# Kernel tuning notes

Hardware: AMD Instinct MI355X
Metric: run time of the kernel (lower is better)

Reference implementation:

```python
import jax, jax.numpy as jnp
import numpy as np

N_NODES = 100000
N_EDGES = 1600000
IN_FT = 128
OUT_FT = 128


def setup_inputs() -> dict:
    key = jax.random.key(0)
    k1, k2, k3, k4, k5, k6 = jax.random.split(key, 6)
    stdv = 1.0 / np.sqrt(OUT_FT)
    x = jax.random.normal(k1, (N_NODES, IN_FT), dtype=jnp.float32)
    edge_rows = jax.random.randint(k2, (N_EDGES,), 0, N_NODES, dtype=jnp.int32)
    edge_cols = jax.random.randint(k3, (N_EDGES,), 0, N_NODES, dtype=jnp.int32)
    # normalized adjacency values (positive, like D^-1 A)
    edge_vals = jax.random.uniform(k4, (N_EDGES,), dtype=jnp.float32)
    W = jax.random.uniform(k5, (IN_FT, OUT_FT), dtype=jnp.float32, minval=-stdv, maxval=stdv)
    b = jax.random.uniform(k6, (OUT_FT,), dtype=jnp.float32, minval=-stdv, maxval=stdv)
    return {"x": x, "edge_rows": edge_rows, "edge_cols": edge_cols,
            "edge_vals": edge_vals, "W": W, "b": b}


def reference(x, edge_rows, edge_cols, edge_vals, W, b):
    # dense projection + bias: [N, out_ft]
    h = x @ W + b
    # SpMM: out[r] = sum_e vals[e] * h[cols[e]] for edges with rows[e] == r
    msgs = edge_vals[:, None] * h[edge_cols]          # [E, out_ft]
    out = jax.ops.segment_sum(msgs, edge_rows, num_segments=N_NODES)
    return jax.nn.relu(out)
```

## Files before the change

kernel.cpp:

```cpp
#include <hip/hip_runtime.h>

#define N_NODES 100000
#define N_EDGES 1600000
#define FT 128

#define NBUCK 391
#define EPB 4096
#define NBLKP ((N_EDGES + EPB - 1) / EPB)
#define CAP 1536
#define CAPB 4800
#define OVFCAP 65536
#define GEMM_BLOCKS ((N_NODES + 255) / 256)
#define SPMM_GRID (8 * 4 * ((NBUCK + 7) / 8))

#define OFF_H 0
#define OFF_BUCKETED 25600000
#define OFF_GCUR 40614400
#define OFF_NOVF 40615964
#define OFF_OVFREC 40615968
#define OFF_OVFBUCK 41140256
#define WS_NEEDED 41402400

typedef __attribute__((ext_vector_type(8))) short bf16x8;
typedef __attribute__((ext_vector_type(4))) float f32x4;

static __device__ __forceinline__ ushort f2bf(float f) {
  const unsigned u = __float_as_uint(f);
  return (ushort)((u + 0x7FFF + ((u >> 16) & 1)) >> 16);
}
static __device__ __forceinline__ float bf2f(ushort s) {
  return __uint_as_float((unsigned)s << 16);
}

__global__ __launch_bounds__(256) void fused_gemm_partC_kernel(
    const float* __restrict__ x,
    const float* __restrict__ W,
    const float* __restrict__ b,
    ushort* __restrict__ h,
    const int* __restrict__ erows,
    const int* __restrict__ ecols,
    const float* __restrict__ evals,
    int* gcur,
    int* novf,
    int2* __restrict__ ovf_rec,
    int* __restrict__ ovf_buck,
    int2* __restrict__ bucketed) {
  __shared__ __align__(16) ushort whi[16384];
  __shared__ int cnt[NBUCK];
  const int tid = threadIdx.x;

  if (blockIdx.x < GEMM_BLOCKS) {
    for (int idx = tid; idx < 16384; idx += 256) {
      const int k = idx >> 7;
      const int col = idx & 127;
      const ushort hi = f2bf(W[idx]);
      const int lane_ = (((k >> 3) & 3) << 4) | (col & 15);
      const int pos =
          ((((k >> 5) << 3) + (col >> 4)) * 64 + lane_) * 8 + (k & 7);
      whi[pos] = hi;
    }
    __syncthreads();

    const int w = tid >> 6;
    const int lane = tid & 63;
    const int r0 = blockIdx.x * 256 + w * 64;
    const int arow = lane & 15;
    const int kgrp = (lane >> 4) << 3;

    float bias_v[8];
#pragma unroll
    for (int ct = 0; ct < 8; ++ct) bias_v[ct] = b[ct * 16 + (lane & 15)];

    f32x4 acc[4][8];
#pragma unroll
    for (int rf = 0; rf < 4; ++rf)
#pragma unroll
      for (int ct = 0; ct < 8; ++ct) acc[rf][ct] = (f32x4){0.f, 0.f, 0.f, 0.f};

#pragma unroll
    for (int ks = 0; ks < 4; ++ks) {
      bf16x8 afr[4];
#pragma unroll
      for (int rf = 0; rf < 4; ++rf) {
        int r = r0 + rf * 16 + arow;
        r = (r < N_NODES) ? r : (N_NODES - 1);
        const float* xp = x + (size_t)r * FT + ks * 32 + kgrp;
        const float4 u0 = *(const float4*)xp;
        const float4 u1 = *(const float4*)(xp + 4);
        bf16x8 a;
        a[0] = (short)f2bf(u0.x);
        a[1] = (short)f2bf(u0.y);
        a[2] = (short)f2bf(u0.z);
        a[3] = (short)f2bf(u0.w);
        a[4] = (short)f2bf(u1.x);
        a[5] = (short)f2bf(u1.y);
        a[6] = (short)f2bf(u1.z);
        a[7] = (short)f2bf(u1.w);
        afr[rf] = a;
      }
#pragma unroll
      for (int ct = 0; ct < 8; ++ct) {
        const int fo = ((ks * 8 + ct) * 64 + lane) * 8;
        const bf16x8 bh = *(const bf16x8*)&whi[fo];
#pragma unroll
        for (int rf = 0; rf < 4; ++rf) {
          acc[rf][ct] = __builtin_amdgcn_mfma_f32_16x16x32_bf16(
              afr[rf], bh, acc[rf][ct], 0, 0, 0);
        }
      }
    }

    const int crow0 = (lane >> 4) << 2;
    const int ccol = lane & 15;
#pragma unroll
    for (int rf = 0; rf < 4; ++rf) {
#pragma unroll
      for (int ct = 0; ct < 8; ++ct) {
        const int col = ct * 16 + ccol;
#pragma unroll
        for (int i = 0; i < 4; ++i) {
          const int row = r0 + rf * 16 + crow0 + i;
          if (row < N_NODES)
            h[(size_t)row * FT + col] = f2bf(acc[rf][ct][i] + bias_v[ct]);
        }
      }
    }
  } else {
    const int bid = blockIdx.x - GEMM_BLOCKS;
    for (int j = tid; j < NBUCK; j += 256) cnt[j] = 0;
    __syncthreads();

    const int base4 = bid * (EPB / 4);
#pragma unroll
    for (int it = 0; it < EPB / 4 / 256; ++it) {
      const int idx4 = base4 + it * 256 + tid;
      if (idx4 < N_EDGES / 4) {
        const int4 r = ((const int4*)erows)[idx4];
        atomicAdd(&cnt[r.x >> 8], 1);
        atomicAdd(&cnt[r.y >> 8], 1);
        atomicAdd(&cnt[r.z >> 8], 1);
        atomicAdd(&cnt[r.w >> 8], 1);
      }
    }
    __syncthreads();

    for (int j = tid; j < NBUCK; j += 256) {
      const int hj = cnt[j];
      int base = 0;
      if (hj > 0) base = atomicAdd(&gcur[j], hj);
      cnt[j] = j * CAPB + ((base < CAPB) ? base : CAPB);
    }
    __syncthreads();

#pragma unroll
    for (int it = 0; it < EPB / 4 / 256; ++it) {
      const int idx4 = base4 + it * 256 + tid;
      if (idx4 < N_EDGES / 4) {
        const int4 r = ((const int4*)erows)[idx4];
        const int4 c = ((const int4*)ecols)[idx4];
        const float4 v = ((const float4*)evals)[idx4];
        int bb, p, lim;
        int2 rec;
#define SCAT(RR, CC, VV)                                           \
        bb = (RR) >> 8;                                            \
        rec.x = (((RR) & 255) << 24) | (CC);                       \
        rec.y = __float_as_int(VV);                                \
        p = atomicAdd(&cnt[bb], 1);                                \
        lim = bb * CAPB + CAPB;                                    \
        if (p < lim) {                                             \
          bucketed[p] = rec;                                       \
        } else {                                                   \
          const int op = atomicAdd(novf, 1);                       \
          if (op < OVFCAP) { ovf_rec[op] = rec; ovf_buck[op] = bb; } \
        }
        SCAT(r.x, c.x, v.x)
        SCAT(r.y, c.y, v.y)
        SCAT(r.z, c.z, v.z)
        SCAT(r.w, c.w, v.w)
#undef SCAT
      }
    }
  }
}

__global__ __launch_bounds__(512) void spmm_bucket_kernel(
    const int2* __restrict__ bucketed,
    const int* __restrict__ gcur,
    const int* __restrict__ novf,
    const int2* __restrict__ ovf_rec,
    const int* __restrict__ ovf_buck,
    const ushort* __restrict__ h,
    float* __restrict__ out) {
  __shared__ int2 tmp[CAP];
  __shared__ int2 eds[CAP];
  __shared__ int cnt[64];
  __shared__ int pos[64];
  __shared__ int cur[64];
  __shared__ int ns;
  const int p_ = blockIdx.x;
  const int x_ = p_ & 7;
  const int m_ = p_ >> 3;
  const int q = m_ & 3;
  const int b = 8 * (m_ >> 2) + x_;
  if (b >= NBUCK) return;
  const int t = threadIdx.x;
  const int beg = b * CAPB;
  const int fill = gcur[b];
  const int end = beg + ((fill < CAPB) ? fill : CAPB);
  const int nov = *novf;

  if (t < 64) cnt[t] = 0;
  if (t == 0) ns = 0;
  __syncthreads();

  for (int i = beg + t; i < end; i += 512) {
    const int2 rec = bucketed[i];
    const int r8 = ((unsigned)rec.x) >> 24;
    if ((r8 >> 6) == q) {
      const int p = atomicAdd(&ns, 1);
      if (p < CAP) {
        tmp[p] = rec;
        atomicAdd(&cnt[r8 & 63], 1);
      }
    }
  }
  __syncthreads();

  const int m = (ns < CAP) ? ns : CAP;
  const bool overflow = (ns > CAP);

  if (t < 64) pos[t] = cnt[t];
  __syncthreads();
#pragma unroll
  for (int d = 1; d < 64; d <<= 1) {
    int u = 0;
    if (t < 64 && t >= d) u = pos[t - d];
    __syncthreads();
    if (t < 64) pos[t] += u;
    __syncthreads();
  }
  if (t < 64) {
    const int excl = pos[t] - cnt[t];
    pos[t] = excl;
    cur[t] = excl;
  }
  __syncthreads();

  for (int i = t; i < m; i += 512) {
    const int2 rec = tmp[i];
    const int r6 = (((unsigned)rec.x) >> 24) & 63;
    const int p = atomicAdd(&cur[r6], 1);
    eds[p] = (int2){rec.x & 0x00FFFFFF, rec.y};
  }
  __syncthreads();

  const int g = t >> 5;
  const int lane = t & 31;
  const int j = lane * 4;

  for (int rr = 0; rr < 4; ++rr) {
    const int r = rr * 16 + g;
    const int row = b * 256 + q * 64 + r;
    const int rbeg = pos[r];
    const int rend = cur[r];

    float a0 = 0.f, a1 = 0.f, a2 = 0.f, a3 = 0.f;
    int e = rbeg;
    for (; e + 3 < rend; e += 4) {
      const int2 p0 = eds[e];
      const int2 p1 = eds[e + 1];
      const int2 p2 = eds[e + 2];
      const int2 p3 = eds[e + 3];
      const ushort4 q0 = *(const ushort4*)(h + (size_t)p0.x * FT + j);
      const ushort4 q1 = *(const ushort4*)(h + (size_t)p1.x * FT + j);
      const ushort4 q2 = *(const ushort4*)(h + (size_t)p2.x * FT + j);
      const ushort4 q3 = *(const ushort4*)(h + (size_t)p3.x * FT + j);
      const float v0 = __int_as_float(p0.y);
      const float v1 = __int_as_float(p1.y);
      const float v2 = __int_as_float(p2.y);
      const float v3 = __int_as_float(p3.y);
      a0 = fmaf(v0, bf2f(q0.x), a0);
      a1 = fmaf(v0, bf2f(q0.y), a1);
      a2 = fmaf(v0, bf2f(q0.z), a2);
      a3 = fmaf(v0, bf2f(q0.w), a3);
      a0 = fmaf(v1, bf2f(q1.x), a0);
      a1 = fmaf(v1, bf2f(q1.y), a1);
      a2 = fmaf(v1, bf2f(q1.z), a2);
      a3 = fmaf(v1, bf2f(q1.w), a3);
      a0 = fmaf(v2, bf2f(q2.x), a0);
      a1 = fmaf(v2, bf2f(q2.y), a1);
      a2 = fmaf(v2, bf2f(q2.z), a2);
      a3 = fmaf(v2, bf2f(q2.w), a3);
      a0 = fmaf(v3, bf2f(q3.x), a0);
      a1 = fmaf(v3, bf2f(q3.y), a1);
      a2 = fmaf(v3, bf2f(q3.z), a2);
      a3 = fmaf(v3, bf2f(q3.w), a3);
    }
    for (; e < rend; ++e) {
      const int2 p0 = eds[e];
      const float v0 = __int_as_float(p0.y);
      const ushort4 q0 = *(const ushort4*)(h + (size_t)p0.x * FT + j);
      a0 = fmaf(v0, bf2f(q0.x), a0);
      a1 = fmaf(v0, bf2f(q0.y), a1);
      a2 = fmaf(v0, bf2f(q0.z), a2);
      a3 = fmaf(v0, bf2f(q0.w), a3);
    }
    if (overflow) {
      int seen = 0;
      const int have = rend - rbeg;
      for (int i = beg; i < end; ++i) {
        const int2 rec = bucketed[i];
        const int r8 = ((unsigned)rec.x) >> 24;
        if ((r8 >> 6) == q && (r8 & 63) == r) {
          ++seen;
          if (seen > have) {
            const float v0 = __int_as_float(rec.y);
            const ushort4 q0 =
                *(const ushort4*)(h + (size_t)(rec.x & 0x00FFFFFF) * FT + j);
            a0 = fmaf(v0, bf2f(q0.x), a0);
            a1 = fmaf(v0, bf2f(q0.y), a1);
            a2 = fmaf(v0, bf2f(q0.z), a2);
            a3 = fmaf(v0, bf2f(q0.w), a3);
          }
        }
      }
    }
    if (nov > 0) {
      const int lim = (nov < OVFCAP) ? nov : OVFCAP;
      for (int i = 0; i < lim; ++i) {
        if (ovf_buck[i] == b) {
          const int2 rec = ovf_rec[i];
          const int r8 = ((unsigned)rec.x) >> 24;
          if ((r8 >> 6) == q && (r8 & 63) == r) {
            const float v0 = __int_as_float(rec.y);
            const ushort4 q0 =
                *(const ushort4*)(h + (size_t)(rec.x & 0x00FFFFFF) * FT + j);
            a0 = fmaf(v0, bf2f(q0.x), a0);
            a1 = fmaf(v0, bf2f(q0.y), a1);
            a2 = fmaf(v0, bf2f(q0.z), a2);
            a3 = fmaf(v0, bf2f(q0.w), a3);
          }
        }
      }
    }

    if (row < N_NODES) {
      float4 o;
      o.x = fmaxf(a0, 0.f);
      o.y = fmaxf(a1, 0.f);
      o.z = fmaxf(a2, 0.f);
      o.w = fmaxf(a3, 0.f);
      *(float4*)(out + (size_t)row * FT + j) = o;
    }
  }
}

__global__ __launch_bounds__(256) void gemm_bias_kernel(
    const float* __restrict__ x,
    const float* __restrict__ W,
    const float* __restrict__ b,
    ushort* __restrict__ h) {
  __shared__ __align__(16) ushort whi[16384];
  const int tid = threadIdx.x;

  for (int idx = tid; idx < 16384; idx += 256) {
    const int k = idx >> 7;
    const int col = idx & 127;
    const ushort hi = f2bf(W[idx]);
    const int lane_ = (((k >> 3) & 3) << 4) | (col & 15);
    const int pos = ((((k >> 5) << 3) + (col >> 4)) * 64 + lane_) * 8 + (k & 7);
    whi[pos] = hi;
  }
  __syncthreads();

  const int w = tid >> 6;
  const int lane = tid & 63;
  const int r0 = blockIdx.x * 256 + w * 64;
  const int arow = lane & 15;
  const int kgrp = (lane >> 4) << 3;

  float bias_v[8];
#pragma unroll
  for (int ct = 0; ct < 8; ++ct) bias_v[ct] = b[ct * 16 + (lane & 15)];

  f32x4 acc[4][8];
#pragma unroll
  for (int rf = 0; rf < 4; ++rf)
#pragma unroll
    for (int ct = 0; ct < 8; ++ct) acc[rf][ct] = (f32x4){0.f, 0.f, 0.f, 0.f};

#pragma unroll
  for (int ks = 0; ks < 4; ++ks) {
    bf16x8 afr[4];
#pragma unroll
    for (int rf = 0; rf < 4; ++rf) {
      int r = r0 + rf * 16 + arow;
      r = (r < N_NODES) ? r : (N_NODES - 1);
      const float* xp = x + (size_t)r * FT + ks * 32 + kgrp;
      const float4 u0 = *(const float4*)xp;
      const float4 u1 = *(const float4*)(xp + 4);
      bf16x8 a;
      a[0] = (short)f2bf(u0.x);
      a[1] = (short)f2bf(u0.y);
      a[2] = (short)f2bf(u0.z);
      a[3] = (short)f2bf(u0.w);
      a[4] = (short)f2bf(u1.x);
      a[5] = (short)f2bf(u1.y);
      a[6] = (short)f2bf(u1.z);
      a[7] = (short)f2bf(u1.w);
      afr[rf] = a;
    }
#pragma unroll
    for (int ct = 0; ct < 8; ++ct) {
      const int fo = ((ks * 8 + ct) * 64 + lane) * 8;
      const bf16x8 bh = *(const bf16x8*)&whi[fo];
#pragma unroll
      for (int rf = 0; rf < 4; ++rf) {
        acc[rf][ct] = __builtin_amdgcn_mfma_f32_16x16x32_bf16(
            afr[rf], bh, acc[rf][ct], 0, 0, 0);
      }
    }
  }

  const int crow0 = (lane >> 4) << 2;
  const int ccol = lane & 15;
#pragma unroll
  for (int rf = 0; rf < 4; ++rf) {
#pragma unroll
    for (int ct = 0; ct < 8; ++ct) {
      const int col = ct * 16 + ccol;
#pragma unroll
      for (int i = 0; i < 4; ++i) {
        const int row = r0 + rf * 16 + crow0 + i;
        if (row < N_NODES)
          h[(size_t)row * FT + col] = f2bf(acc[rf][ct][i] + bias_v[ct]);
      }
    }
  }
}

__global__ __launch_bounds__(256) void edge_scatter_kernel(
    const int* __restrict__ erows,
    const int* __restrict__ ecols,
    const float* __restrict__ evals,
    const ushort* __restrict__ h,
    float* out) {
  const int tid = threadIdx.x;
  const int e = blockIdx.x * 8 + (tid >> 5);
  if (e >= N_EDGES) return;
  const int r = erows[e];
  const int c = ecols[e];
  const float v = evals[e];
  const int j = (tid & 31) * 4;
  const ushort4 q = *(const ushort4*)(h + (size_t)c * FT + j);
  float* op = out + (size_t)r * FT + j;
  atomicAdd(op + 0, v * bf2f(q.x));
  atomicAdd(op + 1, v * bf2f(q.y));
  atomicAdd(op + 2, v * bf2f(q.z));
  atomicAdd(op + 3, v * bf2f(q.w));
}

__global__ __launch_bounds__(256) void relu_kernel(float* out, int n4) {
  const int i = blockIdx.x * blockDim.x + threadIdx.x;
  if (i < n4) {
    float4 v = ((float4*)out)[i];
    v.x = fmaxf(v.x, 0.f);
    v.y = fmaxf(v.y, 0.f);
    v.z = fmaxf(v.z, 0.f);
    v.w = fmaxf(v.w, 0.f);
    ((float4*)out)[i] = v;
  }
}

extern "C" void kernel_launch(void* const* d_in, const int* in_sizes, int n_in,
                              void* d_out, int out_size, void* d_ws, size_t ws_size,
                              hipStream_t stream) {
  const float* x = (const float*)d_in[0];
  const int* erows = (const int*)d_in[1];
  const int* ecols = (const int*)d_in[2];
  const float* evals = (const float*)d_in[3];
  const float* W = (const float*)d_in[4];
  const float* b = (const float*)d_in[5];
  float* out = (float*)d_out;

  char* ws = (char*)d_ws;
  ushort* h = (ushort*)(ws + OFF_H);

  if (ws_size >= (size_t)WS_NEEDED) {
    int2* bucketed = (int2*)(ws + OFF_BUCKETED);
    int* gcur = (int*)(ws + OFF_GCUR);
    int* novf = (int*)(ws + OFF_NOVF);
    int2* ovf_rec = (int2*)(ws + OFF_OVFREC);
    int* ovf_buck = (int*)(ws + OFF_OVFBUCK);

    hipMemsetAsync(gcur, 0, (NBUCK + 1) * sizeof(int), stream);
    fused_gemm_partC_kernel<<<GEMM_BLOCKS + NBLKP, 256, 0, stream>>>(
        x, W, b, h, erows, ecols, evals, gcur, novf, ovf_rec, ovf_buck,
        bucketed);
    spmm_bucket_kernel<<<SPMM_GRID, 512, 0, stream>>>(
        bucketed, gcur, novf, ovf_rec, ovf_buck, h, out);
  } else {
    gemm_bias_kernel<<<GEMM_BLOCKS, 256, 0, stream>>>(x, W, b, h);
    hipMemsetAsync(d_out, 0, (size_t)out_size * sizeof(float), stream);
    edge_scatter_kernel<<<(N_EDGES + 7) / 8, 256, 0, stream>>>(erows, ecols,
                                                               evals, h, out);
    const int n4 = out_size / 4;
    relu_kernel<<<(n4 + 255) / 256, 256, 0, stream>>>(out, n4);
  }
}
```

Baseline: 107.2 us.

## Stage bucketed edges in LDS and write them out contiguously per bucket

The partition blocks now sort each 4096-edge chunk into LDS by bucket, using a block-wide prefix scan over the bucket counts. They then write each bucket's records to global memory as contiguous runs, found with a binary search, instead of scattering every edge straight to global memory. The aim is coalesced global writes instead of random 8-byte scatters. The row indices are kept in registers so erows is not read twice. The cost is a larger LDS footprint (a union with the GEMM weight tile), extra barriers for the scan, and a 9-step binary search per record.

```diff
diff --git a/kernel.cpp b/kernel.cpp
--- a/kernel.cpp
+++ b/kernel.cpp
@@ -31,6 +31,16 @@
 static __device__ __forceinline__ float bf2f(ushort s) {
   return __uint_as_float((unsigned)s << 16);
 }
+
+union SharedU {
+  ushort whi[16384];
+  struct {
+    int2 stage[EPB];
+    int loc[NBUCK + 1];
+    int cur[NBUCK];
+    int gbase[NBUCK];
+  } pc;
+};
 
 __global__ __launch_bounds__(256) void fused_gemm_partC_kernel(
     const float* __restrict__ x,
@@ -45,8 +55,7 @@
     int2* __restrict__ ovf_rec,
     int* __restrict__ ovf_buck,
     int2* __restrict__ bucketed) {
-  __shared__ __align__(16) ushort whi[16384];
-  __shared__ int cnt[NBUCK];
+  __shared__ SharedU shm;
   const int tid = threadIdx.x;
 
   if (blockIdx.x < GEMM_BLOCKS) {
@@ -57,7 +66,7 @@
       const int lane_ = (((k >> 3) & 3) << 4) | (col & 15);
       const int pos =
           ((((k >> 5) << 3) + (col >> 4)) * 64 + lane_) * 8 + (k & 7);
-      whi[pos] = hi;
+      shm.whi[pos] = hi;
     }
     __syncthreads();
 
@@ -101,7 +110,7 @@
 #pragma unroll
       for (int ct = 0; ct < 8; ++ct) {
         const int fo = ((ks * 8 + ct) * 64 + lane) * 8;
-        const bf16x8 bh = *(const bf16x8*)&whi[fo];
+        const bf16x8 bh = *(const bf16x8*)&shm.whi[fo];
 #pragma unroll
         for (int rf = 0; rf < 4; ++rf) {
           acc[rf][ct] = __builtin_amdgcn_mfma_f32_16x16x32_bf16(
@@ -127,57 +136,95 @@
     }
   } else {
     const int bid = blockIdx.x - GEMM_BLOCKS;
-    for (int j = tid; j < NBUCK; j += 256) cnt[j] = 0;
+    for (int j = tid; j < NBUCK; j += 256) shm.pc.cur[j] = 0;
     __syncthreads();
 
     const int base4 = bid * (EPB / 4);
+    int4 rreg[EPB / 4 / 256];
+#pragma unroll
+    for (int it = 0; it < EPB / 4 / 256; ++it) {
+      const int idx4 = base4 + it * 256 + tid;
+      int4 r = {N_NODES, N_NODES, N_NODES, N_NODES};
+      if (idx4 < N_EDGES / 4) {
+        r = ((const int4*)erows)[idx4];
+        atomicAdd(&shm.pc.cur[r.x >> 8], 1);
+        atomicAdd(&shm.pc.cur[r.y >> 8], 1);
+        atomicAdd(&shm.pc.cur[r.z >> 8], 1);
+        atomicAdd(&shm.pc.cur[r.w >> 8], 1);
+      }
+      rreg[it] = r;
+    }
+    __syncthreads();
+
+    for (int j = tid; j < NBUCK; j += 256) {
+      const int hj = shm.pc.cur[j];
+      shm.pc.gbase[j] = (hj > 0) ? atomicAdd(&gcur[j], hj) : 0;
+    }
+
+    {
+      __shared__ int ps[256];
+      const int b0 = tid * 2;
+      int c0 = (b0 < NBUCK) ? shm.pc.cur[b0] : 0;
+      int c1 = (b0 + 1 < NBUCK) ? shm.pc.cur[b0 + 1] : 0;
+      ps[tid] = c0 + c1;
+      __syncthreads();
+#pragma unroll
+      for (int d = 1; d < 256; d <<= 1) {
+        const int u = (tid >= d) ? ps[tid - d] : 0;
+        __syncthreads();
+        ps[tid] += u;
+        __syncthreads();
+      }
+      int run = (tid == 0) ? 0 : ps[tid - 1];
+      if (b0 < NBUCK) shm.pc.loc[b0] = run;
+      run += c0;
+      if (b0 + 1 < NBUCK) shm.pc.loc[b0 + 1] = run;
+      if (tid == 255) shm.pc.loc[NBUCK] = ps[255];
+    }
+    __syncthreads();
+    for (int j = tid; j < NBUCK; j += 256) shm.pc.cur[j] = shm.pc.loc[j];
+    __syncthreads();
+
 #pragma unroll
     for (int it = 0; it < EPB / 4 / 256; ++it) {
       const int idx4 = base4 + it * 256 + tid;
       if (idx4 < N_EDGES / 4) {
-        const int4 r = ((const int4*)erows)[idx4];
-        atomicAdd(&cnt[r.x >> 8], 1);
-        atomicAdd(&cnt[r.y >> 8], 1);
-        atomicAdd(&cnt[r.z >> 8], 1);
-        atomicAdd(&cnt[r.w >> 8], 1);
-      }
-    }
-    __syncthreads();
-
-    for (int j = tid; j < NBUCK; j += 256) {
-      const int hj = cnt[j];
-      int base = 0;
-      if (hj > 0) base = atomicAdd(&gcur[j], hj);
-      cnt[j] = j * CAPB + ((base < CAPB) ? base : CAPB);
-    }
-    __syncthreads();
-
-#pragma unroll
-    for (int it = 0; it < EPB / 4 / 256; ++it) {
-      const int idx4 = base4 + it * 256 + tid;
-      if (idx4 < N_EDGES / 4) {
-        const int4 r = ((const int4*)erows)[idx4];
+        const int4 r = rreg[it];
         const int4 c = ((const int4*)ecols)[idx4];
         const float4 v = ((const float4*)evals)[idx4];
-        int bb, p, lim;
+        int bb, p;
         int2 rec;
-#define SCAT(RR, CC, VV)                                           \
-        bb = (RR) >> 8;                                            \
-        rec.x = (((RR) & 255) << 24) | (CC);                       \
-        rec.y = __float_as_int(VV);                                \
-        p = atomicAdd(&cnt[bb], 1);                                \
-        lim = bb * CAPB + CAPB;                                    \
-        if (p < lim) {                                             \
-          bucketed[p] = rec;                                       \
-        } else {                                                   \
-          const int op = atomicAdd(novf, 1);                       \
-          if (op < OVFCAP) { ovf_rec[op] = rec; ovf_buck[op] = bb; } \
-        }
-        SCAT(r.x, c.x, v.x)
-        SCAT(r.y, c.y, v.y)
-        SCAT(r.z, c.z, v.z)
-        SCAT(r.w, c.w, v.w)
-#undef SCAT
+#define STG(RR, CC, VV)                                  \
+        bb = (RR) >> 8;                                  \
+        rec.x = (((RR) & 255) << 24) | (CC);             \
+        rec.y = __float_as_int(VV);                      \
+        p = atomicAdd(&shm.pc.cur[bb], 1);               \
+        shm.pc.stage[p] = rec;
+        STG(r.x, c.x, v.x)
+        STG(r.y, c.y, v.y)
+        STG(r.z, c.z, v.z)
+        STG(r.w, c.w, v.w)
+#undef STG
+      }
+    }
+    __syncthreads();
+
+    const int total = shm.pc.loc[NBUCK];
+    for (int i = tid; i < total; i += 256) {
+      int lo = 0, hi = NBUCK - 1;
+#pragma unroll
+      for (int s = 0; s < 9; ++s) {
+        const int mid = (lo + hi + 1) >> 1;
+        if (shm.pc.loc[mid] <= i) lo = mid; else hi = mid - 1;
+      }
+      const int bb = lo;
+      const int gp = shm.pc.gbase[bb] + (i - shm.pc.loc[bb]);
+      const int2 rec = shm.pc.stage[i];
+      if (gp < CAPB) {
+        bucketed[(size_t)bb * CAPB + gp] = rec;
+      } else {
+        const int op = atomicAdd(novf, 1);
+        if (op < OVFCAP) { ovf_rec[op] = rec; ovf_buck[op] = bb; }
       }
     }
   }
```

After: 112.3 us. 1.05x slower.
